# Kernel optimization log

Measured on AMD Instinct MI355X. Metric: run time of the kernel, lower is better.

The kernel has to match this reference:

```python
import jax, jax.numpy as jnp
import numpy as np

NEG_INF = -1e30  # stand-in for float('-inf') that is softmax-safe


def setup_inputs() -> dict:
    key = jax.random.key(0)
    ks = jax.random.split(key, 6)
    B, H, S, D = 2, 8, 1024, 64
    NF, K = 4, 3
    return {
        "query": jax.random.normal(ks[0], (B, H, S, D), dtype=jnp.float32),
        "keys": jax.random.normal(ks[1], (B, H, S, D), dtype=jnp.float32),
        "vals": jax.random.normal(ks[2], (B, H, S, D), dtype=jnp.float32),
        "mask": jnp.ones((B, 1, S, S), dtype=jnp.int32),
        "conv_w": jax.random.normal(ks[3], (NF, 1, K, K), dtype=jnp.float32) * (1.0 / K),
        "conv_b": jnp.zeros((NF,), dtype=jnp.float32),
        "lin_w": jax.random.normal(ks[4], (1, NF), dtype=jnp.float32) * 0.5,
        "lin_b": jnp.zeros((1,), dtype=jnp.float32),
    }


def reference(query, keys, vals, mask, conv_w, conv_b, lin_w, lin_b):
    B, H, S, D = query.shape
    NF = conv_w.shape[0]
    K = conv_w.shape[2]
    scale = jnp.asarray(D, query.dtype) ** 0.5

    # [B,H,S,S] raw dot-product scores
    dp = jnp.einsum("bhsd,bhtd->bhst", query, keys) / scale

    # conv2d over the score matrix: treat (B*H) as batch, 1 input channel
    x = dp.reshape(B * H, 1, S, S)
    conv = jax.lax.conv_general_dilated(
        x, conv_w,
        window_strides=(1, 1),
        padding=[(K // 2, K // 2), (K // 2, K // 2)],
        dimension_numbers=("NCHW", "OIHW", "NCHW"),
    ) + conv_b[None, :, None, None]
    conv = jax.nn.leaky_relu(conv, negative_slope=0.01)  # [B*H, NF, S, S]

    # per-pixel linear over the filter axis (Linear(num_filters, 1))
    conv = conv.reshape(B, H, NF, S, S)
    preattn = jnp.einsum("bhfst,f->bhst", conv, lin_w[0]) + lin_b[0]

    # masking + softmax (mask broadcasts over heads)
    preattn = jnp.where(mask == 0, jnp.asarray(NEG_INF, preattn.dtype), preattn)
    attn = jax.nn.softmax(preattn, axis=-1)

    # dropout is identity in eval mode
    return jnp.einsum("bhst,bhtd->bhsd", attn, vals)
```

## Files before the change

### kernel.cpp

```cpp
#include <hip/hip_runtime.h>
#include <math.h>

#define S_LEN 1024
#define D_DIM 64
#define NBH   16
#define RPB   14
#define NSB   74

typedef unsigned short ushort_t;
typedef unsigned int uint_t;
typedef __attribute__((ext_vector_type(8))) short short8;
typedef __attribute__((ext_vector_type(4))) short short4v;
typedef __attribute__((ext_vector_type(4))) float f32x4;
typedef __attribute__((ext_vector_type(2))) float f32x2;
typedef __attribute__((ext_vector_type(2))) _Float16 h2;

__device__ __forceinline__ ushort_t rne_bf16(float x) {
    unsigned u = __float_as_uint(x);
    return (ushort_t)((u + 0x7FFFu + ((u >> 16) & 1u)) >> 16);
}
__device__ __forceinline__ void split1(float x, ushort_t& h, ushort_t& l) {
    h = rne_bf16(x);
    float hf = __uint_as_float((unsigned)h << 16);
    l = rne_bf16(x - hf);
}
__device__ __forceinline__ ushort_t f16bits(float x) {
    _Float16 h = (_Float16)x;
    ushort_t b;
    __builtin_memcpy(&b, &h, 2);
    return b;
}
__device__ __forceinline__ float h2f(ushort_t b) {
    _Float16 h;
    __builtin_memcpy(&h, &b, 2);
    return (float)h;
}
__device__ __forceinline__ h2 as_h2(uint_t u) {
    h2 r;
    __builtin_memcpy(&r, &u, 4);
    return r;
}

__global__ __launch_bounds__(256) void prep(
    const float* __restrict__ k, const float* __restrict__ v,
    const int* __restrict__ mask,
    ushort_t* __restrict__ khi, ushort_t* __restrict__ klo,
    ushort_t* __restrict__ vhi, ushort_t* __restrict__ vlo,
    unsigned* __restrict__ mw)
{
    __shared__ float Ls[64][65];
    const int tid = threadIdx.x;
    const int bx = blockIdx.x;
    if (bx < 512) {
        const int gid  = bx * 256 + tid;
        const int bh   = gid >> 13;
        const int tile = (gid >> 7) & 63;
        const int ch   = (gid >> 6) & 1;
        const int lane = gid & 63;
        const int quad = lane >> 4, t15 = lane & 15;
        const float* src = k + ((size_t)bh * S_LEN + tile * 16 + t15) * D_DIM
                             + ch * 32 + quad * 8;
        float x[8];
        *(float4*)(x + 0) = *(const float4*)(src);
        *(float4*)(x + 4) = *(const float4*)(src + 4);
        short8 hv, lv;
        #pragma unroll
        for (int i = 0; i < 8; ++i) {
            ushort_t h, l;
            split1(x[i], h, l);
            hv[i] = (short)h; lv[i] = (short)l;
        }
        *(short8*)(khi + (size_t)gid * 8) = hv;
        *(short8*)(klo + (size_t)gid * 8) = lv;
    } else if (bx < 768) {
        const int bi = bx - 512;
        const int tt = bi & 15, bh = bi >> 4;
        const float* vb = v + ((size_t)bh * S_LEN + tt * 64) * D_DIM;
        #pragma unroll
        for (int p = 0; p < 4; ++p) {
            int idx = p * 1024 + tid * 4;
            int r = idx >> 6, c = idx & 63;
            float4 x = *(const float4*)(vb + r * 64 + c);
            Ls[r][c] = x.x; Ls[r][c+1] = x.y; Ls[r][c+2] = x.z; Ls[r][c+3] = x.w;
        }
        __syncthreads();
        const int d = tid >> 2, c0 = (tid & 3) * 16;
        ushort_t hi[16], lo[16];
        #pragma unroll
        for (int j = 0; j < 16; ++j) split1(Ls[c0 + j][d], hi[j], lo[j]);
        const int tb0 = tt * 8 + (c0 >> 3);
        const size_t o0 = (((size_t)bh * 128 + tb0) * 64 + d) * 8;
        const size_t o1 = (((size_t)bh * 128 + tb0 + 1) * 64 + d) * 8;
        *(short8*)(vhi + o0) = *(short8*)(hi);
        *(short8*)(vhi + o1) = *(short8*)(hi + 8);
        *(short8*)(vlo + o0) = *(short8*)(lo);
        *(short8*)(vlo + o1) = *(short8*)(lo + 8);
    } else {
        const int gid = (bx - 768) * 256 + tid;
        const int row = gid >> 5, wd = gid & 31;
        const int4* mp = (const int4*)(mask + (size_t)row * 1024 + wd * 32);
        unsigned bits = 0;
        #pragma unroll
        for (int p = 0; p < 8; ++p) {
            int4 qv = mp[p];
            bits |= (qv.x != 0 ? 1u : 0u) << (p * 4 + 0);
            bits |= (qv.y != 0 ? 1u : 0u) << (p * 4 + 1);
            bits |= (qv.z != 0 ? 1u : 0u) << (p * 4 + 2);
            bits |= (qv.w != 0 ? 1u : 0u) << (p * 4 + 3);
        }
        mw[(size_t)row * 32 + wd] = bits;
    }
}

#define DPSTR 1040
#define PSTR  1048
__global__ __launch_bounds__(512) void fused_qk_conv_av(
    const float* __restrict__ q,
    const ushort_t* __restrict__ khi, const ushort_t* __restrict__ klo,
    const unsigned* __restrict__ mw,
    const ushort_t* __restrict__ vhi, const ushort_t* __restrict__ vlo,
    const float* __restrict__ conv_w, const float* __restrict__ conv_b,
    const float* __restrict__ lin_w, const float* __restrict__ lin_b,
    float* __restrict__ out)
{
    __shared__ ushort_t dpH[16 * DPSTR];
    __shared__ ushort_t pP[16 * PSTR];
    __shared__ float oBuf[16][68];
    __shared__ float lsPart[16][4];
    __shared__ unsigned mb[16][32];

    const int st = blockIdx.x, bh = blockIdx.y;
    const int s0 = st * RPB;
    const int b  = bh >> 3;
    const int tid = threadIdx.x;
    const int wave = tid >> 6, lane = tid & 63;
    const int m = lane & 15, quad = lane >> 4;

    {
        const int o = tid >> 5, wd = tid & 31;
        const int s = s0 - 1 + o;
        mb[o][wd] = (s >= 0 && s < S_LEN)
                  ? mw[((size_t)b * S_LEN + s) * 32 + wd] : 0u;
    }

    const int sA = s0 - 1 + m;
    const int sQ = sA < 0 ? 0 : (sA > S_LEN - 1 ? S_LEN - 1 : sA);
    const float* qp = q + ((size_t)bh * S_LEN + sQ) * D_DIM + quad * 8;
    float qa[16];
    *(float4*)(qa + 0)  = *(const float4*)(qp + 0);
    *(float4*)(qa + 4)  = *(const float4*)(qp + 4);
    *(float4*)(qa + 8)  = *(const float4*)(qp + 32);
    *(float4*)(qa + 12) = *(const float4*)(qp + 36);
    short8 AH0, AH1, AL0, AL1;
    #pragma unroll
    for (int i = 0; i < 8; ++i) {
        ushort_t h, l;
        split1(qa[i] * 0.125f, h, l);      AH0[i] = (short)h; AL0[i] = (short)l;
        split1(qa[8 + i] * 0.125f, h, l);  AH1[i] = (short)h; AL1[i] = (short)l;
    }

    #pragma unroll
    for (int tt = 0; tt < 8; ++tt) {
        const int tile = wave * 8 + tt;
        const size_t kb = (((size_t)bh * 64 + tile) * 128 + lane) * 8;
        short8 KH0 = *(const short8*)(khi + kb);
        short8 KL0 = *(const short8*)(klo + kb);
        short8 KH1 = *(const short8*)(khi + kb + 512);
        short8 KL1 = *(const short8*)(klo + kb + 512);
        f32x4 a0 = {0.f, 0.f, 0.f, 0.f}, a1 = {0.f, 0.f, 0.f, 0.f};
        a0 = __builtin_amdgcn_mfma_f32_16x16x32_bf16(AH0, KH0, a0, 0, 0, 0);
        a1 = __builtin_amdgcn_mfma_f32_16x16x32_bf16(AH1, KH1, a1, 0, 0, 0);
        a0 = __builtin_amdgcn_mfma_f32_16x16x32_bf16(AH0, KL0, a0, 0, 0, 0);
        a1 = __builtin_amdgcn_mfma_f32_16x16x32_bf16(AH1, KL1, a1, 0, 0, 0);
        a0 = __builtin_amdgcn_mfma_f32_16x16x32_bf16(AL0, KH0, a0, 0, 0, 0);
        a1 = __builtin_amdgcn_mfma_f32_16x16x32_bf16(AL1, KH1, a1, 0, 0, 0);
        const int col = tile * 16 + m;
        #pragma unroll
        for (int r = 0; r < 4; ++r) {
            const int row = quad * 4 + r;
            const int s = s0 - 1 + row;
            const float v = (s >= 0 && s < S_LEN) ? a0[r] + a1[r] : 0.f;
            dpH[row * DPSTR + col] = f16bits(v);
        }
    }

    float w[36];
    #pragma unroll
    for (int i = 0; i < 36; ++i) w[i] = conv_w[i];
    float cb[4], lw[4];
    #pragma unroll
    for (int f = 0; f < 4; ++f) { cb[f] = conv_b[f]; lw[f] = lin_w[f]; }
    const float lb = lin_b[0];
    const f32x2 zero2 = {0.f, 0.f};
    const f32x2 c001  = {0.01f, 0.01f};

    __syncthreads();

    const int rh = tid >> 8, cg = tid & 255, c0 = cg * 4;
    #pragma unroll
    for (int pass = 0; pass < 2; ++pass) {
        const int obase = rh * 8 + pass * 4;
        float rowv[6][6];
        #pragma unroll
        for (int jj = 0; jj < 6; ++jj) {
            const int dr = obase - 1 + jj;
            if (dr >= 0 && dr < 16) {
                const ushort_t* rp = &dpH[dr * DPSTR + c0];
                uint2 dd = *(const uint2*)rp;
                h2 p0 = as_h2(dd.x), p1 = as_h2(dd.y);
                rowv[jj][0] = cg ? h2f(rp[-1]) : 0.f;
                rowv[jj][1] = (float)p0[0]; rowv[jj][2] = (float)p0[1];
                rowv[jj][3] = (float)p1[0]; rowv[jj][4] = (float)p1[1];
                rowv[jj][5] = (cg < 255) ? h2f(rp[4]) : 0.f;
            } else {
                #pragma unroll
                for (int i = 0; i < 6; ++i) rowv[jj][i] = 0.f;
            }
        }
        float ls[4];
        #pragma unroll
        for (int jo = 0; jo < 4; ++jo) {
            const int o = obase + jo;
            const bool act = (o >= 1) && (o <= RPB) && (s0 - 1 + o < S_LEN);
            if (act) {
                f32x2 pa = {lb, lb}, pb = {lb, lb};
                #pragma unroll
                for (int f = 0; f < 4; ++f) {
                    f32x2 ca = {cb[f], cb[f]}, cbv = ca;
                    #pragma unroll
                    for (int dr = 0; dr < 3; ++dr) {
                        const float* vv = rowv[jo + dr];
                        #pragma unroll
                        for (int dc = 0; dc < 3; ++dc) {
                            const float wt = w[f * 9 + dr * 3 + dc];
                            const f32x2 wt2 = {wt, wt};
                            f32x2 ia = {vv[dc],     vv[dc + 1]};
                            f32x2 ib = {vv[dc + 2], vv[dc + 3]};
                            ca  = __builtin_elementwise_fma(wt2, ia, ca);
                            cbv = __builtin_elementwise_fma(wt2, ib, cbv);
                        }
                    }
                    const f32x2 lwv = {lw[f], lw[f]};
                    f32x2 la  = __builtin_elementwise_fma(
                        c001, __builtin_elementwise_min(ca, zero2),
                        __builtin_elementwise_max(ca, zero2));
                    f32x2 lb2 = __builtin_elementwise_fma(
                        c001, __builtin_elementwise_min(cbv, zero2),
                        __builtin_elementwise_max(cbv, zero2));
                    pa = __builtin_elementwise_fma(lwv, la, pa);
                    pb = __builtin_elementwise_fma(lwv, lb2, pb);
                }
                const unsigned word = mb[o][cg >> 3];
                const unsigned nib  = (word >> ((cg & 7) * 4)) & 0xFu;
                float pre[4] = {pa.x, pa.y, pb.x, pb.y};
                #pragma unroll
                for (int i = 0; i < 4; ++i)
                    if (!((nib >> i) & 1u)) pre[i] = -1e30f;
                float pv[4];
                #pragma unroll
                for (int i = 0; i < 4; ++i) pv[i] = __expf(pre[i]);
                ls[jo] = (pv[0] + pv[1]) + (pv[2] + pv[3]);
                short4v hv = {(short)rne_bf16(pv[0]), (short)rne_bf16(pv[1]),
                              (short)rne_bf16(pv[2]), (short)rne_bf16(pv[3])};
                *(short4v*)&pP[o * PSTR + c0] = hv;
            } else {
                short4v z = {0, 0, 0, 0};
                *(short4v*)&pP[o * PSTR + c0] = z;
                ls[jo] = 0.f;
            }
        }
        #pragma unroll
        for (int jo = 0; jo < 4; ++jo) {
            float t = ls[jo];
            #pragma unroll
            for (int off = 1; off < 64; off <<= 1) t += __shfl_xor(t, off);
            if (lane == 0) lsPart[obase + jo][wave & 3] = t;
        }
    }
    __syncthreads();

    const int d0 = (wave & 3) * 16;
    const int th = wave >> 2;
    f32x4 O = {0.f, 0.f, 0.f, 0.f};
    #pragma unroll 4
    for (int i = 0; i < 16; ++i) {
        const int c = th * 16 + i;
        short8 ph = *(const short8*)&pP[m * PSTR + c * 32 + quad * 8];
        const size_t vb = (((size_t)bh * 128 + c * 4 + quad) * 64 + d0 + m) * 8;
        short8 vh = *(const short8*)(vhi + vb);
        short8 vl = *(const short8*)(vlo + vb);
        O = __builtin_amdgcn_mfma_f32_16x16x32_bf16(ph, vh, O, 0, 0, 0);
        O = __builtin_amdgcn_mfma_f32_16x16x32_bf16(ph, vl, O, 0, 0, 0);
    }
    if (wave < 4) {
        #pragma unroll
        for (int r = 0; r < 4; ++r) oBuf[quad * 4 + r][d0 + m] = O[r];
    }
    __syncthreads();
    if (wave >= 4) {
        #pragma unroll
        for (int r = 0; r < 4; ++r) {
            const int br = quad * 4 + r;
            const int s = s0 - 1 + br;
            if (br >= 1 && br <= RPB && s < S_LEN) {
                const float lsum = (lsPart[br][0] + lsPart[br][1]) +
                                   (lsPart[br][2] + lsPart[br][3]);
                out[((size_t)bh * S_LEN + s) * D_DIM + d0 + m] =
                    (O[r] + oBuf[br][d0 + m]) / lsum;
            }
        }
    }
}

extern "C" void kernel_launch(void* const* d_in, const int* in_sizes, int n_in,
                              void* d_out, int out_size, void* d_ws, size_t ws_size,
                              hipStream_t stream) {
    const float* q      = (const float*)d_in[0];
    const float* k      = (const float*)d_in[1];
    const float* v      = (const float*)d_in[2];
    const int*   mask   = (const int*)d_in[3];
    const float* conv_w = (const float*)d_in[4];
    const float* conv_b = (const float*)d_in[5];
    const float* lin_w  = (const float*)d_in[6];
    const float* lin_b  = (const float*)d_in[7];
    float* out = (float*)d_out;

    char* wsb = (char*)d_ws;
    const size_t MB = 1024 * 1024;
    ushort_t* khi = (ushort_t*)(wsb + 0 * MB);
    ushort_t* klo = (ushort_t*)(wsb + 2 * MB);
    ushort_t* vhi = (ushort_t*)(wsb + 4 * MB);
    ushort_t* vlo = (ushort_t*)(wsb + 6 * MB);
    unsigned* mw  = (unsigned*)(wsb + 8 * MB);

    prep<<<dim3(1024), 256, 0, stream>>>(k, v, mask, khi, klo, vhi, vlo, mw);
    fused_qk_conv_av<<<dim3(NSB, NBH), 512, 0, stream>>>(
        q, khi, klo, mw, vhi, vlo, conv_w, conv_b, lin_w, lin_b, out);
}
```

Measured before the change: 131.4 us.

## Replace split-bf16 MFMA with single fp16 MFMA and pad score rows

Replaces the hi/lo bf16 split emulation of fp32 (three MFMAs for QK, two for PV) with a single fp16 operand per matrix, so one MFMA per product replaces three or two. K and V workspace traffic is halved, and the prep kernel does less conversion work. The score buffer now carries two zero-padded columns on each side, which removes the edge branches and scalar halo loads in the conv stencil. The risk is precision: fp16 has fewer mantissa bits than split bf16 and can overflow on large values, so outputs may drift from the fp32 reference.

```diff
diff --git a/kernel.cpp b/kernel.cpp
--- a/kernel.cpp
+++ b/kernel.cpp
@@ -9,32 +9,18 @@
 
 typedef unsigned short ushort_t;
 typedef unsigned int uint_t;
-typedef __attribute__((ext_vector_type(8))) short short8;
+typedef __attribute__((ext_vector_type(8))) _Float16 half8;
+typedef __attribute__((ext_vector_type(2))) _Float16 h2;
 typedef __attribute__((ext_vector_type(4))) short short4v;
 typedef __attribute__((ext_vector_type(4))) float f32x4;
 typedef __attribute__((ext_vector_type(2))) float f32x2;
-typedef __attribute__((ext_vector_type(2))) _Float16 h2;
-
-__device__ __forceinline__ ushort_t rne_bf16(float x) {
-    unsigned u = __float_as_uint(x);
-    return (ushort_t)((u + 0x7FFFu + ((u >> 16) & 1u)) >> 16);
-}
-__device__ __forceinline__ void split1(float x, ushort_t& h, ushort_t& l) {
-    h = rne_bf16(x);
-    float hf = __uint_as_float((unsigned)h << 16);
-    l = rne_bf16(x - hf);
-}
+
 __device__ __forceinline__ ushort_t f16bits(float x) {
     _Float16 h = (_Float16)x;
     ushort_t b;
     __builtin_memcpy(&b, &h, 2);
     return b;
 }
-__device__ __forceinline__ float h2f(ushort_t b) {
-    _Float16 h;
-    __builtin_memcpy(&h, &b, 2);
-    return (float)h;
-}
 __device__ __forceinline__ h2 as_h2(uint_t u) {
     h2 r;
     __builtin_memcpy(&r, &u, 4);
@@ -44,8 +30,7 @@
 __global__ __launch_bounds__(256) void prep(
     const float* __restrict__ k, const float* __restrict__ v,
     const int* __restrict__ mask,
-    ushort_t* __restrict__ khi, ushort_t* __restrict__ klo,
-    ushort_t* __restrict__ vhi, ushort_t* __restrict__ vlo,
+    ushort_t* __restrict__ kh, ushort_t* __restrict__ vh,
     unsigned* __restrict__ mw)
 {
     __shared__ float Ls[64][65];
@@ -63,15 +48,11 @@
         float x[8];
         *(float4*)(x + 0) = *(const float4*)(src);
         *(float4*)(x + 4) = *(const float4*)(src + 4);
-        short8 hv, lv;
-        #pragma unroll
-        for (int i = 0; i < 8; ++i) {
-            ushort_t h, l;
-            split1(x[i], h, l);
-            hv[i] = (short)h; lv[i] = (short)l;
-        }
-        *(short8*)(khi + (size_t)gid * 8) = hv;
-        *(short8*)(klo + (size_t)gid * 8) = lv;
+        ushort_t hv[8];
+        #pragma unroll
+        for (int i = 0; i < 8; ++i) hv[i] = f16bits(x[i]);
+        *(short4v*)(kh + (size_t)gid * 8)     = *(short4v*)(hv);
+        *(short4v*)(kh + (size_t)gid * 8 + 4) = *(short4v*)(hv + 4);
     } else if (bx < 768) {
         const int bi = bx - 512;
         const int tt = bi & 15, bh = bi >> 4;
@@ -85,16 +66,16 @@
         }
         __syncthreads();
         const int d = tid >> 2, c0 = (tid & 3) * 16;
-        ushort_t hi[16], lo[16];
-        #pragma unroll
-        for (int j = 0; j < 16; ++j) split1(Ls[c0 + j][d], hi[j], lo[j]);
+        ushort_t hi[16];
+        #pragma unroll
+        for (int j = 0; j < 16; ++j) hi[j] = f16bits(Ls[c0 + j][d]);
         const int tb0 = tt * 8 + (c0 >> 3);
         const size_t o0 = (((size_t)bh * 128 + tb0) * 64 + d) * 8;
         const size_t o1 = (((size_t)bh * 128 + tb0 + 1) * 64 + d) * 8;
-        *(short8*)(vhi + o0) = *(short8*)(hi);
-        *(short8*)(vhi + o1) = *(short8*)(hi + 8);
-        *(short8*)(vlo + o0) = *(short8*)(lo);
-        *(short8*)(vlo + o1) = *(short8*)(lo + 8);
+        *(short4v*)(vh + o0)     = *(short4v*)(hi);
+        *(short4v*)(vh + o0 + 4) = *(short4v*)(hi + 4);
+        *(short4v*)(vh + o1)     = *(short4v*)(hi + 8);
+        *(short4v*)(vh + o1 + 4) = *(short4v*)(hi + 12);
     } else {
         const int gid = (bx - 768) * 256 + tid;
         const int row = gid >> 5, wd = gid & 31;
@@ -116,9 +97,8 @@
 #define PSTR  1048
 __global__ __launch_bounds__(512) void fused_qk_conv_av(
     const float* __restrict__ q,
-    const ushort_t* __restrict__ khi, const ushort_t* __restrict__ klo,
-    const unsigned* __restrict__ mw,
-    const ushort_t* __restrict__ vhi, const ushort_t* __restrict__ vlo,
+    const ushort_t* __restrict__ kh, const unsigned* __restrict__ mw,
+    const ushort_t* __restrict__ vh,
     const float* __restrict__ conv_w, const float* __restrict__ conv_b,
     const float* __restrict__ lin_w, const float* __restrict__ lin_b,
     float* __restrict__ out)
@@ -142,6 +122,11 @@
         mb[o][wd] = (s >= 0 && s < S_LEN)
                   ? mw[((size_t)b * S_LEN + s) * 32 + wd] : 0u;
     }
+    if (tid < 64) {
+        const int row = tid >> 2, i = tid & 3;
+        const int idx = (i < 2) ? i : 1024 + i;
+        dpH[row * DPSTR + idx] = 0;
+    }
 
     const int sA = s0 - 1 + m;
     const int sQ = sA < 0 ? 0 : (sA > S_LEN - 1 ? S_LEN - 1 : sA);
@@ -151,36 +136,29 @@
     *(float4*)(qa + 4)  = *(const float4*)(qp + 4);
     *(float4*)(qa + 8)  = *(const float4*)(qp + 32);
     *(float4*)(qa + 12) = *(const float4*)(qp + 36);
-    short8 AH0, AH1, AL0, AL1;
+    half8 AH0, AH1;
     #pragma unroll
     for (int i = 0; i < 8; ++i) {
-        ushort_t h, l;
-        split1(qa[i] * 0.125f, h, l);      AH0[i] = (short)h; AL0[i] = (short)l;
-        split1(qa[8 + i] * 0.125f, h, l);  AH1[i] = (short)h; AL1[i] = (short)l;
+        AH0[i] = (_Float16)(qa[i] * 0.125f);
+        AH1[i] = (_Float16)(qa[8 + i] * 0.125f);
     }
 
     #pragma unroll
     for (int tt = 0; tt < 8; ++tt) {
         const int tile = wave * 8 + tt;
         const size_t kb = (((size_t)bh * 64 + tile) * 128 + lane) * 8;
-        short8 KH0 = *(const short8*)(khi + kb);
-        short8 KL0 = *(const short8*)(klo + kb);
-        short8 KH1 = *(const short8*)(khi + kb + 512);
-        short8 KL1 = *(const short8*)(klo + kb + 512);
-        f32x4 a0 = {0.f, 0.f, 0.f, 0.f}, a1 = {0.f, 0.f, 0.f, 0.f};
-        a0 = __builtin_amdgcn_mfma_f32_16x16x32_bf16(AH0, KH0, a0, 0, 0, 0);
-        a1 = __builtin_amdgcn_mfma_f32_16x16x32_bf16(AH1, KH1, a1, 0, 0, 0);
-        a0 = __builtin_amdgcn_mfma_f32_16x16x32_bf16(AH0, KL0, a0, 0, 0, 0);
-        a1 = __builtin_amdgcn_mfma_f32_16x16x32_bf16(AH1, KL1, a1, 0, 0, 0);
-        a0 = __builtin_amdgcn_mfma_f32_16x16x32_bf16(AL0, KH0, a0, 0, 0, 0);
-        a1 = __builtin_amdgcn_mfma_f32_16x16x32_bf16(AL1, KH1, a1, 0, 0, 0);
+        half8 KH0 = *(const half8*)(kh + kb);
+        half8 KH1 = *(const half8*)(kh + kb + 512);
+        f32x4 a = {0.f, 0.f, 0.f, 0.f};
+        a = __builtin_amdgcn_mfma_f32_16x16x32_f16(AH0, KH0, a, 0, 0, 0);
+        a = __builtin_amdgcn_mfma_f32_16x16x32_f16(AH1, KH1, a, 0, 0, 0);
         const int col = tile * 16 + m;
         #pragma unroll
         for (int r = 0; r < 4; ++r) {
             const int row = quad * 4 + r;
             const int s = s0 - 1 + row;
-            const float v = (s >= 0 && s < S_LEN) ? a0[r] + a1[r] : 0.f;
-            dpH[row * DPSTR + col] = f16bits(v);
+            const float v = (s >= 0 && s < S_LEN) ? a[r] : 0.f;
+            dpH[row * DPSTR + col + 2] = f16bits(v);
         }
     }
 
@@ -206,12 +184,14 @@
             const int dr = obase - 1 + jj;
             if (dr >= 0 && dr < 16) {
                 const ushort_t* rp = &dpH[dr * DPSTR + c0];
-                uint2 dd = *(const uint2*)rp;
-                h2 p0 = as_h2(dd.x), p1 = as_h2(dd.y);
-                rowv[jj][0] = cg ? h2f(rp[-1]) : 0.f;
-                rowv[jj][1] = (float)p0[0]; rowv[jj][2] = (float)p0[1];
-                rowv[jj][3] = (float)p1[0]; rowv[jj][4] = (float)p1[1];
-                rowv[jj][5] = (cg < 255) ? h2f(rp[4]) : 0.f;
+                uint2 r0 = *(const uint2*)rp;
+                uint2 r1 = *(const uint2*)(rp + 4);
+                h2 pA = as_h2(r0.x), pB = as_h2(r0.y);
+                h2 pC = as_h2(r1.x), pD = as_h2(r1.y);
+                rowv[jj][0] = (float)pA[1];
+                rowv[jj][1] = (float)pB[0]; rowv[jj][2] = (float)pB[1];
+                rowv[jj][3] = (float)pC[0]; rowv[jj][4] = (float)pC[1];
+                rowv[jj][5] = (float)pD[0];
             } else {
                 #pragma unroll
                 for (int i = 0; i < 6; ++i) rowv[jj][i] = 0.f;
@@ -260,12 +240,13 @@
                 #pragma unroll
                 for (int i = 0; i < 4; ++i) pv[i] = __expf(pre[i]);
                 ls[jo] = (pv[0] + pv[1]) + (pv[2] + pv[3]);
-                short4v hv = {(short)rne_bf16(pv[0]), (short)rne_bf16(pv[1]),
-                              (short)rne_bf16(pv[2]), (short)rne_bf16(pv[3])};
-                *(short4v*)&pP[o * PSTR + c0] = hv;
+                uint2 hv;
+                hv.x = (uint_t)f16bits(pv[0]) | ((uint_t)f16bits(pv[1]) << 16);
+                hv.y = (uint_t)f16bits(pv[2]) | ((uint_t)f16bits(pv[3]) << 16);
+                *(uint2*)&pP[o * PSTR + c0] = hv;
             } else {
-                short4v z = {0, 0, 0, 0};
-                *(short4v*)&pP[o * PSTR + c0] = z;
+                uint2 z = {0u, 0u};
+                *(uint2*)&pP[o * PSTR + c0] = z;
                 ls[jo] = 0.f;
             }
         }
@@ -285,12 +266,10 @@
     #pragma unroll 4
     for (int i = 0; i < 16; ++i) {
         const int c = th * 16 + i;
-        short8 ph = *(const short8*)&pP[m * PSTR + c * 32 + quad * 8];
+        half8 ph = *(const half8*)&pP[m * PSTR + c * 32 + quad * 8];
         const size_t vb = (((size_t)bh * 128 + c * 4 + quad) * 64 + d0 + m) * 8;
-        short8 vh = *(const short8*)(vhi + vb);
-        short8 vl = *(const short8*)(vlo + vb);
-        O = __builtin_amdgcn_mfma_f32_16x16x32_bf16(ph, vh, O, 0, 0, 0);
-        O = __builtin_amdgcn_mfma_f32_16x16x32_bf16(ph, vl, O, 0, 0, 0);
+        half8 vv = *(const half8*)(vh + vb);
+        O = __builtin_amdgcn_mfma_f32_16x16x32_f16(ph, vv, O, 0, 0, 0);
     }
     if (wave < 4) {
         #pragma unroll
@@ -327,13 +306,11 @@
 
     char* wsb = (char*)d_ws;
     const size_t MB = 1024 * 1024;
-    ushort_t* khi = (ushort_t*)(wsb + 0 * MB);
-    ushort_t* klo = (ushort_t*)(wsb + 2 * MB);
-    ushort_t* vhi = (ushort_t*)(wsb + 4 * MB);
-    ushort_t* vlo = (ushort_t*)(wsb + 6 * MB);
-    unsigned* mw  = (unsigned*)(wsb + 8 * MB);
-
-    prep<<<dim3(1024), 256, 0, stream>>>(k, v, mask, khi, klo, vhi, vlo, mw);
+    ushort_t* kh = (ushort_t*)(wsb + 0 * MB);
+    ushort_t* vh = (ushort_t*)(wsb + 2 * MB);
+    unsigned* mw = (unsigned*)(wsb + 4 * MB);
+
+    prep<<<dim3(1024), 256, 0, stream>>>(k, v, mask, kh, vh, mw);
     fused_qk_conv_av<<<dim3(NSB, NBH), 512, 0, stream>>>(
-        q, khi, klo, mw, vhi, vlo, conv_w, conv_b, lin_w, lin_b, out);
-}
+        q, kh, mw, vh, conv_w, conv_b, lin_w, lin_b, out);
+}
```

Result: faster. 121.6 us (-7.4%).
